# Performance work log

Hardware: AMD Instinct MI355X
Metric: run time of the kernel (lower is better)

## Reference

```python
import jax, jax.numpy as jnp
import numpy as np

L, E, H, FF, N, S, ML = 6, 768, 12, 3072, 8, 1023, 2048


def setup_inputs() -> dict:
    key = jax.random.key(0)
    ks = jax.random.split(key, 16)
    rn = lambda k, shape, s=0.02: jax.random.normal(k, shape, jnp.float32) * s
    return {
        "x": jax.random.normal(ks[0], (N, S, E), jnp.float32),
        "mask": jnp.ones((N, 1, 1, S + 1), jnp.int32),
        "pos_emb": rn(ks[1], (ML, E), 1.0),
        "cls": rn(ks[2], (1, 1, E), 1.0),
        "Wq": rn(ks[3], (L, E, E)), "bq": jnp.zeros((L, E), jnp.float32),
        "Wk": rn(ks[4], (L, E, E)), "bk": jnp.zeros((L, E), jnp.float32),
        "Wv": rn(ks[5], (L, E, E)), "bv": jnp.zeros((L, E), jnp.float32),
        "Wo": rn(ks[6], (L, E, E)), "bo": jnp.zeros((L, E), jnp.float32),
        "ln1_g": jnp.ones((L, E), jnp.float32), "ln1_b": jnp.zeros((L, E), jnp.float32),
        "ln2_g": jnp.ones((L, E), jnp.float32), "ln2_b": jnp.zeros((L, E), jnp.float32),
        "Wf1": rn(ks[7], (L, E, FF)), "bf1": jnp.zeros((L, FF), jnp.float32),
        "Wf2": rn(ks[8], (L, FF, E)), "bf2": jnp.zeros((L, E), jnp.float32),
    }


def _ln(x, g, b, eps=1e-5):
    m = x.mean(-1, keepdims=True)
    v = ((x - m) ** 2).mean(-1, keepdims=True)
    return (x - m) / jnp.sqrt(v + eps) * g + b


def reference(x, mask, pos_emb, cls, Wq, bq, Wk, bk, Wv, bv, Wo, bo,
              ln1_g, ln1_b, ln2_g, ln2_b, Wf1, bf1, Wf2, bf2):
    n, s, e = x.shape
    h = H
    d = e // h
    # prepend CLS token -> [N, T, E], add learned positions
    x = jnp.concatenate([jnp.broadcast_to(cls, (n, 1, e)), x], axis=1)
    t = s + 1
    out = x + pos_emb[:t][None]
    scale = jnp.float32(1.0 / np.sqrt(d))
    for i in range(Wq.shape[0]):
        q = (out @ Wq[i] + bq[i]).reshape(n, t, h, d)
        k = (out @ Wk[i] + bk[i]).reshape(n, t, h, d)
        v = (out @ Wv[i] + bv[i]).reshape(n, t, h, d)
        energy = jnp.einsum('nqhd,nkhd->nhqk', q, k)  # [N,H,T,T]
        energy = jnp.where(mask == 0, jnp.float32(-1e20), energy)
        attn = jax.nn.softmax(energy * scale, axis=-1)
        att = jnp.einsum('nhqk,nkhd->nqhd', attn, v).reshape(n, t, e)
        att = att @ Wo[i] + bo[i]
        hid = _ln(att + out, ln1_g[i], ln1_b[i])  # residual uses query (=out)
        ff = jax.nn.gelu(hid @ Wf1[i] + bf1[i], approximate=False) @ Wf2[i] + bf2[i]
        out = _ln(ff + hid, ln2_g[i], ln2_b[i])
    return out
```

## Files before the change

### kernel.cpp

```cpp
#include <hip/hip_runtime.h>

#define L_ 6
#define E_ 768
#define H_ 12
#define FF_ 3072

typedef __attribute__((ext_vector_type(8))) short bh8;
typedef __attribute__((ext_vector_type(4))) float f32x4;

__device__ inline ushort f2bf(float f) {
  unsigned u = __builtin_bit_cast(unsigned, f);
  u += 0x7fffu + ((u >> 16) & 1u);
  return (ushort)(u >> 16);
}

__device__ __forceinline__ void gload16(const void* g, void* l) {
  __builtin_amdgcn_global_load_lds(
      (const __attribute__((address_space(1))) void*)g,
      (__attribute__((address_space(3))) void*)l, 16, 0, 0);
}

__global__ __launch_bounds__(256) void pack_bias(const float* __restrict__ bq,
                                                 const float* __restrict__ bk,
                                                 const float* __restrict__ bv,
                                                 float* __restrict__ bqkv) {
  int idx = blockIdx.x * 256 + threadIdx.x;
  int l = idx / 2304, j = idx % 2304;
  float v = (j < 768) ? bq[l * 768 + j]
          : (j < 1536) ? bk[l * 768 + j - 768]
                       : bv[l * 768 + j - 1536];
  bqkv[idx] = v;
}

__global__ __launch_bounds__(256) void transpose_w(const float* __restrict__ src,
                                                   ushort* __restrict__ dst,
                                                   int K, int Nn,
                                                   long sstride, long dstride) {
  src += (long)blockIdx.z * sstride;
  dst += (long)blockIdx.z * dstride;
  __shared__ float t[32][33];
  int tx = threadIdx.x & 31, ty = threadIdx.x >> 5;
  int kb = blockIdx.x * 32, nb = blockIdx.y * 32;
#pragma unroll
  for (int i = 0; i < 4; i++) {
    int kr = ty + i * 8;
    t[kr][tx] = src[(long)(kb + kr) * Nn + nb + tx];
  }
  __syncthreads();
#pragma unroll
  for (int i = 0; i < 4; i++) {
    int nr = ty + i * 8;
    dst[(long)(nb + nr) * K + kb + tx] = f2bf(t[tx][nr]);
  }
}

__global__ __launch_bounds__(256) void embed_k(const float* __restrict__ x,
                                               const float* __restrict__ pos,
                                               const float* __restrict__ cls,
                                               float* __restrict__ res,
                                               ushort* __restrict__ xb) {
  int idx = blockIdx.x * 256 + threadIdx.x;
  int c4 = idx % 192;
  int row = idx / 192;
  int t = row & 1023, n = row >> 10;
  f32x4 pv = ((const f32x4*)pos)[t * 192 + c4];
  f32x4 xv;
  if (t == 0) xv = ((const f32x4*)cls)[c4];
  else        xv = ((const f32x4*)x)[(size_t)(n * 1023 + t - 1) * 192 + c4];
  f32x4 s = xv + pv;
  ((f32x4*)res)[idx] = s;
  ushort4 h;
  h.x = f2bf(s[0]); h.y = f2bf(s[1]); h.z = f2bf(s[2]); h.w = f2bf(s[3]);
  ((ushort4*)xb)[idx] = h;
}

template <int MODE>
__global__ __launch_bounds__(256, 4) void gemm_bt(const ushort* __restrict__ A,
                                                  const ushort* __restrict__ Bt,
                                                  int M, int N, int K,
                                                  const float* __restrict__ bias,
                                                  const float* __restrict__ resid,
                                                  float* __restrict__ out32,
                                                  ushort* __restrict__ out16,
                                                  ushort* __restrict__ vtb) {
  __shared__ ushort As[128 * 64];
  __shared__ ushort Bs[128 * 64];
  int tid = threadIdx.x;
  int wid = tid >> 6, lane = tid & 63;
  int wm = wid >> 1, wn = wid & 1;
  int l15 = lane & 15, lhi = lane >> 4;
  int ln8 = lane >> 3, lc8 = (lane & 7) * 8;
  int row0 = blockIdx.x * 128, col0 = blockIdx.y * 128;

  f32x4 acc[4][4];
#pragma unroll
  for (int i = 0; i < 4; i++)
#pragma unroll
    for (int j = 0; j < 4; j++) acc[i][j] = (f32x4){0.f, 0.f, 0.f, 0.f};

  const ushort* Ap = A + (size_t)(row0 + wid * 32 + ln8) * K + lc8;
  const ushort* Bp = Bt + (size_t)(col0 + wid * 32 + ln8) * K + lc8;

  int nt = K >> 6;
  for (int kt = 0; kt < nt; ++kt) {
    int k0 = kt << 6;
#pragma unroll
    for (int p = 0; p < 4; p++) {
      int r = wid * 32 + p * 8;
      gload16(Ap + (size_t)p * 8 * K + k0, As + r * 64);
      gload16(Bp + (size_t)p * 8 * K + k0, Bs + r * 64);
    }
    __syncthreads();
#pragma unroll
    for (int ks = 0; ks < 2; ks++) {
      bh8 af[4], bfr[4];
#pragma unroll
      for (int i = 0; i < 4; i++)
        af[i] = *(const bh8*)(As + (wm * 64 + i * 16 + l15) * 64 + ks * 32 + lhi * 8);
#pragma unroll
      for (int j = 0; j < 4; j++)
        bfr[j] = *(const bh8*)(Bs + (wn * 64 + j * 16 + l15) * 64 + ks * 32 + lhi * 8);
#pragma unroll
      for (int i = 0; i < 4; i++)
#pragma unroll
        for (int j = 0; j < 4; j++)
          acc[i][j] = __builtin_amdgcn_mfma_f32_16x16x32_bf16(af[i], bfr[j], acc[i][j], 0, 0, 0);
    }
    __syncthreads();
  }

#pragma unroll
  for (int j = 0; j < 4; j++) {
    int col = col0 + wn * 64 + j * 16 + l15;
    float bv = bias[col];
#pragma unroll
    for (int i = 0; i < 4; i++) {
      int rbase = row0 + wm * 64 + i * 16 + lhi * 4;
      if (MODE == 0 && col >= 1536) {
        int hd = col - 1536;
        int nn = rbase >> 10, t0 = rbase & 1023;
        ushort4 h4;
        h4.x = f2bf(acc[i][j][0] + bv);
        h4.y = f2bf(acc[i][j][1] + bv);
        h4.z = f2bf(acc[i][j][2] + bv);
        h4.w = f2bf(acc[i][j][3] + bv);
        *(ushort4*)(vtb + ((size_t)nn * 768 + hd) * 1024 + t0) = h4;
      } else {
#pragma unroll
        for (int r = 0; r < 4; r++) {
          int row = rbase + r;
          size_t o = (size_t)row * N + col;
          float v = acc[i][j][r] + bv;
          if (MODE == 0) {
            out16[o] = f2bf(v);
          } else if (MODE == 1) {
            out32[o] = v + resid[o];
          } else {
            v = 0.5f * v * (1.f + erff(v * 0.70710678118f));
            out16[o] = f2bf(v);
          }
        }
      }
    }
  }
}

__global__ __launch_bounds__(256) void attn_k(const ushort* __restrict__ qkv,
                                              const ushort* __restrict__ vtb,
                                              const int* __restrict__ mask,
                                              ushort* __restrict__ attb) {
  int qt = blockIdx.x, h = blockIdx.y, n = blockIdx.z;
  int tid = threadIdx.x, wid = tid >> 6, lane = tid & 63;
  int l15 = lane & 15, lhi = lane >> 4;
  __shared__ ushort Ks[2][64 * 64];
  __shared__ ushort Vs[2][64 * 64];
  __shared__ ushort Pt[4][16 * 64];
  ushort* Pw = Pt[wid];

  int ln8 = lane >> 3;
  int swc = (((lane & 7) ^ ln8) << 3);

  const ushort* Kg = qkv + 768 + h * 64;
  const ushort* Vg = vtb + (size_t)(n * 768 + h * 64) * 1024;

  auto stage = [&](int b, int kv0) {
#pragma unroll
    for (int it = 0; it < 2; ++it) {
      int r = wid * 16 + it * 8;
      gload16(Kg + (size_t)(n * 1024 + kv0 + r + ln8) * 2304 + swc, &Ks[b][r * 64]);
      gload16(Vg + (size_t)(r + ln8) * 1024 + kv0 + swc, &Vs[b][r * 64]);
    }
  };

  stage(0, 0);

  int q0 = qt * 64 + wid * 16;
  size_t rowQ = (size_t)(n * 1024 + q0 + l15) * 2304 + h * 64;
  bh8 qf0 = *(const bh8*)(qkv + rowQ + lhi * 8);
  bh8 qf1 = *(const bh8*)(qkv + rowQ + 32 + lhi * 8);

  unsigned long long mbits = 0ull;
#pragma unroll
  for (int i = 0; i < 64; ++i)
    mbits |= (unsigned long long)(mask[n * 1024 + i * 16 + l15] != 0) << i;

  bh8 ones;
#pragma unroll
  for (int i = 0; i < 8; ++i) ones[i] = (short)0x3F80;

  f32x4 o[4], lacc = (f32x4){0.f, 0.f, 0.f, 0.f};
#pragma unroll
  for (int i = 0; i < 4; i++) o[i] = (f32x4){0.f, 0.f, 0.f, 0.f};

  int x15 = (l15 & 7) << 3;
  int buf = 0;
  for (int t = 0; t < 16; ++t) {
    if (t < 15) {
      stage(buf ^ 1, (t + 1) * 64);
      asm volatile("s_waitcnt vmcnt(4)" ::: "memory");
    } else {
      asm volatile("s_waitcnt vmcnt(0)" ::: "memory");
    }
    __builtin_amdgcn_s_barrier();
    const ushort* Kb = Ks[buf];
    const ushort* Vb = Vs[buf];

    f32x4 s[4];
    __builtin_amdgcn_s_setprio(1);
#pragma unroll
    for (int t4 = 0; t4 < 4; ++t4) {
      int rs = (t4 * 16 + l15) * 64;
      s[t4] = (f32x4){0.f, 0.f, 0.f, 0.f};
      s[t4] = __builtin_amdgcn_mfma_f32_16x16x32_bf16(qf0, *(const bh8*)(Kb + rs + ((lhi << 3) ^ x15)), s[t4], 0, 0, 0);
      s[t4] = __builtin_amdgcn_mfma_f32_16x16x32_bf16(qf1, *(const bh8*)(Kb + rs + (((4 + lhi) << 3) ^ x15)), s[t4], 0, 0, 0);
    }
    __builtin_amdgcn_s_setprio(0);

#pragma unroll
    for (int t4 = 0; t4 < 4; ++t4) {
      bool mk = (mbits >> (t * 4 + t4)) & 1ull;
#pragma unroll
      for (int r = 0; r < 4; r++) {
        float xv = mk ? s[t4][r] * 0.125f : -1e20f;
        float p = __expf(fminf(xv, 80.f));
        int prow = lhi * 4 + r;
        int slot = t4 * 2 + (l15 >> 3);
        Pw[prow * 64 + (((slot ^ (prow & 7)) << 3) | (l15 & 7))] = f2bf(p);
      }
    }

    bh8 pf0 = *(const bh8*)(Pw + l15 * 64 + ((lhi << 3) ^ x15));
    bh8 pf1 = *(const bh8*)(Pw + l15 * 64 + (((4 + lhi) << 3) ^ x15));
    __builtin_amdgcn_s_setprio(1);
#pragma unroll
    for (int nb = 0; nb < 4; nb++) {
      int rs = (nb * 16 + l15) * 64;
      o[nb] = __builtin_amdgcn_mfma_f32_16x16x32_bf16(pf0, *(const bh8*)(Vb + rs + ((lhi << 3) ^ x15)), o[nb], 0, 0, 0);
      o[nb] = __builtin_amdgcn_mfma_f32_16x16x32_bf16(pf1, *(const bh8*)(Vb + rs + (((4 + lhi) << 3) ^ x15)), o[nb], 0, 0, 0);
    }
    lacc = __builtin_amdgcn_mfma_f32_16x16x32_bf16(pf0, ones, lacc, 0, 0, 0);
    lacc = __builtin_amdgcn_mfma_f32_16x16x32_bf16(pf1, ones, lacc, 0, 0, 0);
    __builtin_amdgcn_s_setprio(0);

    if (t < 15) {
      asm volatile("s_waitcnt lgkmcnt(0)" ::: "memory");
      __builtin_amdgcn_s_barrier();
    }
    buf ^= 1;
  }

#pragma unroll
  for (int nb = 0; nb < 4; nb++)
#pragma unroll
    for (int r = 0; r < 4; r++) {
      float val = o[nb][r] / lacc[r];
      int row = q0 + lhi * 4 + r;
      int col = h * 64 + nb * 16 + l15;
      attb[(size_t)(n * 1024 + row) * 768 + col] = f2bf(val);
    }
}

__global__ __launch_bounds__(256) void ln_k(const float* __restrict__ in,
                                            const float* __restrict__ g,
                                            const float* __restrict__ b,
                                            float* __restrict__ y32,
                                            ushort* __restrict__ y16) {
  int row = blockIdx.x, tid = threadIdx.x;
  size_t base = (size_t)row * 768;
  float v0 = in[base + tid], v1 = in[base + tid + 256], v2 = in[base + tid + 512];
  float s = v0 + v1 + v2;
  float sq = v0 * v0 + v1 * v1 + v2 * v2;
#pragma unroll
  for (int off = 32; off > 0; off >>= 1) {
    s += __shfl_down(s, off);
    sq += __shfl_down(sq, off);
  }
  __shared__ float sws[4], swq[4];
  int wid = tid >> 6, lane = tid & 63;
  if (lane == 0) { sws[wid] = s; swq[wid] = sq; }
  __syncthreads();
  float ts = sws[0] + sws[1] + sws[2] + sws[3];
  float tq = swq[0] + swq[1] + swq[2] + swq[3];
  float mean = ts * (1.f / 768.f);
  float var = tq * (1.f / 768.f) - mean * mean;
  float rstd = rsqrtf(var + 1e-5f);
#pragma unroll
  for (int i = 0; i < 3; i++) {
    int c = tid + i * 256;
    float vv = (i == 0) ? v0 : (i == 1) ? v1 : v2;
    float y = (vv - mean) * rstd * g[c] + b[c];
    y32[base + c] = y;
    y16[base + c] = f2bf(y);
  }
}

extern "C" void kernel_launch(void* const* d_in, const int* in_sizes, int n_in,
                              void* d_out, int out_size, void* d_ws, size_t ws_size,
                              hipStream_t stream) {
  const float* x    = (const float*)d_in[0];
  const int*   mask = (const int*)d_in[1];
  const float* pos  = (const float*)d_in[2];
  const float* cls  = (const float*)d_in[3];
  const float* Wq   = (const float*)d_in[4];
  const float* bq   = (const float*)d_in[5];
  const float* Wk   = (const float*)d_in[6];
  const float* bk   = (const float*)d_in[7];
  const float* Wv   = (const float*)d_in[8];
  const float* bv   = (const float*)d_in[9];
  const float* Wo   = (const float*)d_in[10];
  const float* bo   = (const float*)d_in[11];
  const float* ln1g = (const float*)d_in[12];
  const float* ln1b = (const float*)d_in[13];
  const float* ln2g = (const float*)d_in[14];
  const float* ln2b = (const float*)d_in[15];
  const float* Wf1  = (const float*)d_in[16];
  const float* bf1  = (const float*)d_in[17];
  const float* Wf2  = (const float*)d_in[18];
  const float* bf2  = (const float*)d_in[19];

  char* ws = (char*)d_ws;
  size_t off = 0;
  auto alloc = [&](size_t bytes) {
    char* p = ws + off;
    off += (bytes + 255) & ~(size_t)255;
    return p;
  };
  const size_t M = 8192;
  ushort* qkvt = (ushort*)alloc((size_t)L_ * 2304 * 768 * 2);
  ushort* wot  = (ushort*)alloc((size_t)L_ * 768 * 768 * 2);
  ushort* wf1t = (ushort*)alloc((size_t)L_ * 3072 * 768 * 2);
  ushort* wf2t = (ushort*)alloc((size_t)L_ * 768 * 3072 * 2);
  float*  bqkv = (float*)alloc((size_t)L_ * 2304 * 4);
  float*  res  = (float*)alloc(M * 768 * 4);
  float*  pre  = (float*)alloc(M * 768 * 4);
  ushort* xb   = (ushort*)alloc(M * 768 * 2);
  ushort* qkvb = (ushort*)alloc(M * 2304 * 2);
  ushort* vtb  = (ushort*)alloc(M * 768 * 2);
  ushort* attb = (ushort*)alloc(M * 768 * 2);
  ushort* ffb  = (ushort*)alloc(M * 3072 * 2);
  (void)ws_size; (void)in_sizes; (void)n_in; (void)out_size;

  dim3 tb(256);
  pack_bias<<<54, tb, 0, stream>>>(bq, bk, bv, bqkv);
  transpose_w<<<dim3(24, 24, 6), tb, 0, stream>>>(Wq, qkvt,              768, 768, 768L * 768, 2304L * 768);
  transpose_w<<<dim3(24, 24, 6), tb, 0, stream>>>(Wk, qkvt + 768 * 768,  768, 768, 768L * 768, 2304L * 768);
  transpose_w<<<dim3(24, 24, 6), tb, 0, stream>>>(Wv, qkvt + 2 * 768 * 768, 768, 768, 768L * 768, 2304L * 768);
  transpose_w<<<dim3(24, 24, 6), tb, 0, stream>>>(Wo, wot, 768, 768, 768L * 768, 768L * 768);
  transpose_w<<<dim3(24, 96, 6), tb, 0, stream>>>(Wf1, wf1t, 768, 3072, 768L * 3072, 3072L * 768);
  transpose_w<<<dim3(96, 24, 6), tb, 0, stream>>>(Wf2, wf2t, 3072, 768, 3072L * 768, 768L * 3072);
  embed_k<<<6144, tb, 0, stream>>>(x, pos, cls, res, xb);

  for (int l = 0; l < L_; l++) {
    gemm_bt<0><<<dim3(64, 18), tb, 0, stream>>>(xb, qkvt + (size_t)l * 2304 * 768,
                                                8192, 2304, 768, bqkv + l * 2304,
                                                nullptr, nullptr, qkvb, vtb);
    attn_k<<<dim3(16, 12, 8), tb, 0, stream>>>(qkvb, vtb, mask, attb);
    gemm_bt<1><<<dim3(64, 6), tb, 0, stream>>>(attb, wot + (size_t)l * 768 * 768,
                                               8192, 768, 768, bo + l * 768,
                                               res, pre, nullptr, nullptr);
    ln_k<<<8192, tb, 0, stream>>>(pre, ln1g + l * 768, ln1b + l * 768, res, xb);
    gemm_bt<2><<<dim3(64, 24), tb, 0, stream>>>(xb, wf1t + (size_t)l * 3072 * 768,
                                                8192, 3072, 768, bf1 + l * 3072,
                                                nullptr, nullptr, ffb, nullptr);
    gemm_bt<1><<<dim3(64, 6), tb, 0, stream>>>(ffb, wf2t + (size_t)l * 768 * 3072,
                                               8192, 768, 3072, bf2 + l * 768,
                                               res, pre, nullptr, nullptr);
    float* y32 = (l == L_ - 1) ? (float*)d_out : res;
    ln_k<<<8192, tb, 0, stream>>>(pre, ln2g + l * 768, ln2b + l * 768, y32, xb);
  }
}
```

Before: 2.028 ms.

## Split-K the N=768 GEMMs and fuse partial reduction into LayerNorm

Adds a split-K mode to the GEMM that writes four fp32 partial tiles per output, raising the block count for the Wo and FFN2 projections from 384 to 1536. A new LayerNorm kernel sums the partials, adds bias and residual, then normalizes. This targets under-filled CUs on these narrow GEMMs, but adds a large partial buffer and extra global memory traffic. The new path is taken only when the workspace is large enough.

New measurement: 2.030 ms. About the same (+0.1%).

```diff
diff --git a/kernel.cpp b/kernel.cpp
--- a/kernel.cpp
+++ b/kernel.cpp
@@ -82,7 +82,8 @@
                                                   const float* __restrict__ resid,
                                                   float* __restrict__ out32,
                                                   ushort* __restrict__ out16,
-                                                  ushort* __restrict__ vtb) {
+                                                  ushort* __restrict__ vtb,
+                                                  int ksl) {
   __shared__ ushort As[128 * 64];
   __shared__ ushort Bs[128 * 64];
   int tid = threadIdx.x;
@@ -91,6 +92,8 @@
   int l15 = lane & 15, lhi = lane >> 4;
   int ln8 = lane >> 3, lc8 = (lane & 7) * 8;
   int row0 = blockIdx.x * 128, col0 = blockIdx.y * 128;
+  int kb = (MODE == 3) ? blockIdx.z * ksl : 0;
+  int nt = ((MODE == 3) ? ksl : K) >> 6;
 
   f32x4 acc[4][4];
 #pragma unroll
@@ -98,10 +101,9 @@
 #pragma unroll
     for (int j = 0; j < 4; j++) acc[i][j] = (f32x4){0.f, 0.f, 0.f, 0.f};
 
-  const ushort* Ap = A + (size_t)(row0 + wid * 32 + ln8) * K + lc8;
-  const ushort* Bp = Bt + (size_t)(col0 + wid * 32 + ln8) * K + lc8;
-
-  int nt = K >> 6;
+  const ushort* Ap = A + (size_t)(row0 + wid * 32 + ln8) * K + kb + lc8;
+  const ushort* Bp = Bt + (size_t)(col0 + wid * 32 + ln8) * K + kb + lc8;
+
   for (int kt = 0; kt < nt; ++kt) {
     int k0 = kt << 6;
 #pragma unroll
@@ -129,10 +131,11 @@
     __syncthreads();
   }
 
+  float* outp = (MODE == 3) ? out32 + (size_t)blockIdx.z * M * N : out32;
 #pragma unroll
   for (int j = 0; j < 4; j++) {
     int col = col0 + wn * 64 + j * 16 + l15;
-    float bv = bias[col];
+    float bv = (MODE == 3) ? 0.f : bias[col];
 #pragma unroll
     for (int i = 0; i < 4; i++) {
       int rbase = row0 + wm * 64 + i * 16 + lhi * 4;
@@ -155,6 +158,8 @@
             out16[o] = f2bf(v);
           } else if (MODE == 1) {
             out32[o] = v + resid[o];
+          } else if (MODE == 3) {
+            outp[o] = v;
           } else {
             v = 0.5f * v * (1.f + erff(v * 0.70710678118f));
             out16[o] = f2bf(v);
@@ -309,6 +314,50 @@
     int c = tid + i * 256;
     float vv = (i == 0) ? v0 : (i == 1) ? v1 : v2;
     float y = (vv - mean) * rstd * g[c] + b[c];
+    y32[base + c] = y;
+    y16[base + c] = f2bf(y);
+  }
+}
+
+__global__ __launch_bounds__(256) void ln_red_k(const float* __restrict__ part,
+                                                const float* __restrict__ resid,
+                                                const float* __restrict__ bias,
+                                                const float* __restrict__ g,
+                                                const float* __restrict__ b,
+                                                float* __restrict__ y32,
+                                                ushort* __restrict__ y16) {
+  int row = blockIdx.x, tid = threadIdx.x;
+  size_t base = (size_t)row * 768;
+  const size_t sstride = (size_t)8192 * 768;
+  float v[3];
+#pragma unroll
+  for (int i = 0; i < 3; i++) {
+    int c = tid + i * 256;
+    float s = resid[base + c] + bias[c];
+#pragma unroll
+    for (int sl = 0; sl < 4; ++sl) s += part[sl * sstride + base + c];
+    v[i] = s;
+  }
+  float s = v[0] + v[1] + v[2];
+  float sq = v[0] * v[0] + v[1] * v[1] + v[2] * v[2];
+#pragma unroll
+  for (int off = 32; off > 0; off >>= 1) {
+    s += __shfl_down(s, off);
+    sq += __shfl_down(sq, off);
+  }
+  __shared__ float sws[4], swq[4];
+  int wid = tid >> 6, lane = tid & 63;
+  if (lane == 0) { sws[wid] = s; swq[wid] = sq; }
+  __syncthreads();
+  float ts = sws[0] + sws[1] + sws[2] + sws[3];
+  float tq = swq[0] + swq[1] + swq[2] + swq[3];
+  float mean = ts * (1.f / 768.f);
+  float var = tq * (1.f / 768.f) - mean * mean;
+  float rstd = rsqrtf(var + 1e-5f);
+#pragma unroll
+  for (int i = 0; i < 3; i++) {
+    int c = tid + i * 256;
+    float y = (v[i] - mean) * rstd * g[c] + b[c];
     y32[base + c] = y;
     y16[base + c] = f2bf(y);
   }
@@ -358,7 +407,10 @@
   ushort* vtb  = (ushort*)alloc(M * 768 * 2);
   ushort* attb = (ushort*)alloc(M * 768 * 2);
   ushort* ffb  = (ushort*)alloc(M * 3072 * 2);
-  (void)ws_size; (void)in_sizes; (void)n_in; (void)out_size;
+  size_t off_nopart = off;
+  float* part = (float*)alloc((size_t)4 * M * 768 * 4);
+  bool use_split = (off <= ws_size);
+  (void)off_nopart; (void)in_sizes; (void)n_in; (void)out_size;
 
   dim3 tb(256);
   pack_bias<<<54, tb, 0, stream>>>(bq, bk, bv, bqkv);
@@ -373,19 +425,35 @@
   for (int l = 0; l < L_; l++) {
     gemm_bt<0><<<dim3(64, 18), tb, 0, stream>>>(xb, qkvt + (size_t)l * 2304 * 768,
                                                 8192, 2304, 768, bqkv + l * 2304,
-                                                nullptr, nullptr, qkvb, vtb);
+                                                nullptr, nullptr, qkvb, vtb, 0);
     attn_k<<<dim3(16, 12, 8), tb, 0, stream>>>(qkvb, vtb, mask, attb);
-    gemm_bt<1><<<dim3(64, 6), tb, 0, stream>>>(attb, wot + (size_t)l * 768 * 768,
-                                               8192, 768, 768, bo + l * 768,
-                                               res, pre, nullptr, nullptr);
-    ln_k<<<8192, tb, 0, stream>>>(pre, ln1g + l * 768, ln1b + l * 768, res, xb);
+    if (use_split) {
+      gemm_bt<3><<<dim3(64, 6, 4), tb, 0, stream>>>(attb, wot + (size_t)l * 768 * 768,
+                                                    8192, 768, 768, nullptr,
+                                                    nullptr, part, nullptr, nullptr, 192);
+      ln_red_k<<<8192, tb, 0, stream>>>(part, res, bo + l * 768,
+                                        ln1g + l * 768, ln1b + l * 768, res, xb);
+    } else {
+      gemm_bt<1><<<dim3(64, 6), tb, 0, stream>>>(attb, wot + (size_t)l * 768 * 768,
+                                                 8192, 768, 768, bo + l * 768,
+                                                 res, pre, nullptr, nullptr, 0);
+      ln_k<<<8192, tb, 0, stream>>>(pre, ln1g + l * 768, ln1b + l * 768, res, xb);
+    }
     gemm_bt<2><<<dim3(64, 24), tb, 0, stream>>>(xb, wf1t + (size_t)l * 3072 * 768,
                                                 8192, 3072, 768, bf1 + l * 3072,
-                                                nullptr, nullptr, ffb, nullptr);
-    gemm_bt<1><<<dim3(64, 6), tb, 0, stream>>>(ffb, wf2t + (size_t)l * 768 * 3072,
-                                               8192, 768, 3072, bf2 + l * 768,
-                                               res, pre, nullptr, nullptr);
+                                                nullptr, nullptr, ffb, nullptr, 0);
     float* y32 = (l == L_ - 1) ? (float*)d_out : res;
-    ln_k<<<8192, tb, 0, stream>>>(pre, ln2g + l * 768, ln2b + l * 768, y32, xb);
-  }
-}
+    if (use_split) {
+      gemm_bt<3><<<dim3(64, 6, 4), tb, 0, stream>>>(ffb, wf2t + (size_t)l * 768 * 3072,
+                                                    8192, 768, 3072, nullptr,
+                                                    nullptr, part, nullptr, nullptr, 768);
+      ln_red_k<<<8192, tb, 0, stream>>>(part, res, bf2 + l * 768,
+                                        ln2g + l * 768, ln2b + l * 768, y32, xb);
+    } else {
+      gemm_bt<1><<<dim3(64, 6), tb, 0, stream>>>(ffb, wf2t + (size_t)l * 768 * 3072,
+                                                 8192, 768, 3072, bf2 + l * 768,
+                                                 res, pre, nullptr, nullptr, 0);
+      ln_k<<<8192, tb, 0, stream>>>(pre, ln2g + l * 768, ln2b + l * 768, y32, xb);
+    }
+  }
+}
```

## Split-K the output and FF2 GEMMs, reduce partials inside layernorm

Applied to the files above, without the earlier changes.

The N=768 GEMMs (attention output projection and FF2) now run split-K across blockIdx.z: 4 slices for the projection and 3 for FF2. This raises the grid from 384 blocks to 1536 or 1152 so more of the GPU's compute units are busy. Each slice writes fp32 partials into scratch buffers aliased onto pre, qkvb and ffb. The layernorm kernel now sums those partials together with the bias and residual. The cost is extra fp32 partial-sum traffic and relying on those buffers being dead at that point (slD aliases ffb, which is only used in the 4-way split, before FF1 writes ffb).

Result: no change. 2.042 ms (+0.7%).

```diff
diff --git a/kernel.cpp b/kernel.cpp
--- a/kernel.cpp
+++ b/kernel.cpp
@@ -79,10 +79,13 @@
                                                   const ushort* __restrict__ Bt,
                                                   int M, int N, int K,
                                                   const float* __restrict__ bias,
-                                                  const float* __restrict__ resid,
-                                                  float* __restrict__ out32,
+                                                  float* __restrict__ sp0,
+                                                  float* __restrict__ sp1,
+                                                  float* __restrict__ sp2,
+                                                  float* __restrict__ sp3,
                                                   ushort* __restrict__ out16,
-                                                  ushort* __restrict__ vtb) {
+                                                  ushort* __restrict__ vtb,
+                                                  int ksl) {
   __shared__ ushort As[128 * 64];
   __shared__ ushort Bs[128 * 64];
   int tid = threadIdx.x;
@@ -91,6 +94,8 @@
   int l15 = lane & 15, lhi = lane >> 4;
   int ln8 = lane >> 3, lc8 = (lane & 7) * 8;
   int row0 = blockIdx.x * 128, col0 = blockIdx.y * 128;
+  int kb = (MODE == 3) ? blockIdx.z * ksl : 0;
+  int nt = ((MODE == 3) ? ksl : K) >> 6;
 
   f32x4 acc[4][4];
 #pragma unroll
@@ -98,10 +103,9 @@
 #pragma unroll
     for (int j = 0; j < 4; j++) acc[i][j] = (f32x4){0.f, 0.f, 0.f, 0.f};
 
-  const ushort* Ap = A + (size_t)(row0 + wid * 32 + ln8) * K + lc8;
-  const ushort* Bp = Bt + (size_t)(col0 + wid * 32 + ln8) * K + lc8;
-
-  int nt = K >> 6;
+  const ushort* Ap = A + (size_t)(row0 + wid * 32 + ln8) * K + kb + lc8;
+  const ushort* Bp = Bt + (size_t)(col0 + wid * 32 + ln8) * K + kb + lc8;
+
   for (int kt = 0; kt < nt; ++kt) {
     int k0 = kt << 6;
 #pragma unroll
@@ -129,10 +133,13 @@
     __syncthreads();
   }
 
+  float* outp = nullptr;
+  if (MODE == 3)
+    outp = (blockIdx.z == 0) ? sp0 : (blockIdx.z == 1) ? sp1 : (blockIdx.z == 2) ? sp2 : sp3;
 #pragma unroll
   for (int j = 0; j < 4; j++) {
     int col = col0 + wn * 64 + j * 16 + l15;
-    float bv = bias[col];
+    float bv = (MODE == 3) ? 0.f : bias[col];
 #pragma unroll
     for (int i = 0; i < 4; i++) {
       int rbase = row0 + wm * 64 + i * 16 + lhi * 4;
@@ -153,8 +160,8 @@
           float v = acc[i][j][r] + bv;
           if (MODE == 0) {
             out16[o] = f2bf(v);
-          } else if (MODE == 1) {
-            out32[o] = v + resid[o];
+          } else if (MODE == 3) {
+            outp[o] = v;
           } else {
             v = 0.5f * v * (1.f + erff(v * 0.70710678118f));
             out16[o] = f2bf(v);
@@ -280,16 +287,31 @@
     }
 }
 
-__global__ __launch_bounds__(256) void ln_k(const float* __restrict__ in,
-                                            const float* __restrict__ g,
-                                            const float* __restrict__ b,
-                                            float* __restrict__ y32,
-                                            ushort* __restrict__ y16) {
+template <int S>
+__global__ __launch_bounds__(256) void ln_red_k(const float* __restrict__ p0,
+                                                const float* __restrict__ p1,
+                                                const float* __restrict__ p2,
+                                                const float* __restrict__ p3,
+                                                const float* __restrict__ resid,
+                                                const float* __restrict__ bias,
+                                                const float* __restrict__ g,
+                                                const float* __restrict__ b,
+                                                float* __restrict__ y32,
+                                                ushort* __restrict__ y16) {
   int row = blockIdx.x, tid = threadIdx.x;
   size_t base = (size_t)row * 768;
-  float v0 = in[base + tid], v1 = in[base + tid + 256], v2 = in[base + tid + 512];
-  float s = v0 + v1 + v2;
-  float sq = v0 * v0 + v1 * v1 + v2 * v2;
+  float v[3];
+#pragma unroll
+  for (int i = 0; i < 3; i++) {
+    int c = tid + i * 256;
+    float s = resid[base + c] + bias[c];
+    s += p0[base + c] + p1[base + c];
+    if (S > 2) s += p2[base + c];
+    if (S > 3) s += p3[base + c];
+    v[i] = s;
+  }
+  float s = v[0] + v[1] + v[2];
+  float sq = v[0] * v[0] + v[1] * v[1] + v[2] * v[2];
 #pragma unroll
   for (int off = 32; off > 0; off >>= 1) {
     s += __shfl_down(s, off);
@@ -307,8 +329,7 @@
 #pragma unroll
   for (int i = 0; i < 3; i++) {
     int c = tid + i * 256;
-    float vv = (i == 0) ? v0 : (i == 1) ? v1 : v2;
-    float y = (vv - mean) * rstd * g[c] + b[c];
+    float y = (v[i] - mean) * rstd * g[c] + b[c];
     y32[base + c] = y;
     y16[base + c] = f2bf(y);
   }
@@ -360,6 +381,11 @@
   ushort* ffb  = (ushort*)alloc(M * 3072 * 2);
   (void)ws_size; (void)in_sizes; (void)n_in; (void)out_size;
 
+  float* slA = pre;
+  float* slB = (float*)qkvb;
+  float* slC = (float*)((char*)qkvb + M * 768 * 4);
+  float* slD = (float*)ffb;
+
   dim3 tb(256);
   pack_bias<<<54, tb, 0, stream>>>(bq, bk, bv, bqkv);
   transpose_w<<<dim3(24, 24, 6), tb, 0, stream>>>(Wq, qkvt,              768, 768, 768L * 768, 2304L * 768);
@@ -373,19 +399,25 @@
   for (int l = 0; l < L_; l++) {
     gemm_bt<0><<<dim3(64, 18), tb, 0, stream>>>(xb, qkvt + (size_t)l * 2304 * 768,
                                                 8192, 2304, 768, bqkv + l * 2304,
-                                                nullptr, nullptr, qkvb, vtb);
+                                                nullptr, nullptr, nullptr, nullptr,
+                                                qkvb, vtb, 0);
     attn_k<<<dim3(16, 12, 8), tb, 0, stream>>>(qkvb, vtb, mask, attb);
-    gemm_bt<1><<<dim3(64, 6), tb, 0, stream>>>(attb, wot + (size_t)l * 768 * 768,
-                                               8192, 768, 768, bo + l * 768,
-                                               res, pre, nullptr, nullptr);
-    ln_k<<<8192, tb, 0, stream>>>(pre, ln1g + l * 768, ln1b + l * 768, res, xb);
+    gemm_bt<3><<<dim3(64, 6, 4), tb, 0, stream>>>(attb, wot + (size_t)l * 768 * 768,
+                                                  8192, 768, 768, nullptr,
+                                                  slA, slB, slC, slD,
+                                                  nullptr, nullptr, 192);
+    ln_red_k<4><<<8192, tb, 0, stream>>>(slA, slB, slC, slD, res, bo + l * 768,
+                                         ln1g + l * 768, ln1b + l * 768, res, xb);
     gemm_bt<2><<<dim3(64, 24), tb, 0, stream>>>(xb, wf1t + (size_t)l * 3072 * 768,
                                                 8192, 3072, 768, bf1 + l * 3072,
-                                                nullptr, nullptr, ffb, nullptr);
-    gemm_bt<1><<<dim3(64, 6), tb, 0, stream>>>(ffb, wf2t + (size_t)l * 768 * 3072,
-                                               8192, 768, 3072, bf2 + l * 768,
-                                               res, pre, nullptr, nullptr);
+                                                nullptr, nullptr, nullptr, nullptr,
+                                                ffb, nullptr, 0);
     float* y32 = (l == L_ - 1) ? (float*)d_out : res;
-    ln_k<<<8192, tb, 0, stream>>>(pre, ln2g + l * 768, ln2b + l * 768, y32, xb);
-  }
-}
+    gemm_bt<3><<<dim3(64, 6, 3), tb, 0, stream>>>(ffb, wf2t + (size_t)l * 768 * 3072,
+                                                  8192, 768, 3072, nullptr,
+                                                  slA, slB, slC, nullptr,
+                                                  nullptr, nullptr, 1024);
+    ln_red_k<3><<<8192, tb, 0, stream>>>(slA, slB, slC, nullptr, res, bf2 + l * 768,
+                                         ln2g + l * 768, ln2b + l * 768, y32, xb);
+  }
+}
```
